# Performance work log

Measured on AMD Instinct MI355X. Metric: run time of the kernel, lower is better.

Reference implementation:

```python
import jax, jax.numpy as jnp
import numpy as np

NUM_ROUTING = 3


def squash(s, axis=-1):
    # squash(s) = |s|^2/(1+|s|^2) * s/|s|  (no epsilon, matching the torch code)
    sq = jnp.sum(s * s, axis=axis, keepdims=True)
    return sq / (1.0 + sq) * (s / jnp.sqrt(sq))


def setup_inputs() -> dict:
    key = jax.random.key(0)
    k1, k2 = jax.random.split(key)
    B, in_dim, in_num = 256, 8, 1152
    out_num, out_dim = 10, 16
    x = jax.random.normal(k1, (B, in_dim, in_num), dtype=jnp.float32)
    W = jax.random.normal(k2, (in_num, out_num, out_dim, in_dim), dtype=jnp.float32)
    return {"x": x, "W": W}


def reference(x, W):
    # x: [B, in_dim, in_num]; W: [in_num(i), out_num(j), out_dim(d), in_dim(c)]
    B = x.shape[0]
    in_num, out_num = W.shape[0], W.shape[1]
    # u_hat[i,j,b,d] = sum_c W[i,j,d,c] * x[b,c,i]
    u_hat = jnp.einsum('ijdc,bci->ijbd', W, x)
    b_ij = jnp.zeros((in_num, out_num), dtype=x.dtype)
    v = None
    for _ in range(NUM_ROUTING):
        # DGL reduce: softmax over the output-capsule axis (bucket dim)
        c = jax.nn.softmax(b_ij, axis=1)                    # [i, j]
        s = jnp.einsum('ij,ijbd->jbd', c, u_hat)            # [j, B, d]
        v = squash(s, axis=2)                               # [j, B, d]
        # edge update: b_ij += mean_b sum_d v[j,b,d] * u_hat[i,j,b,d]
        b_ij = b_ij + jnp.einsum('jbd,ijbd->ij', v, u_hat) / B
    # output: [B, out_num, out_dim, 1]
    return jnp.transpose(v, (1, 0, 2))[..., None]
```

## Files before the change

### kernel.cpp

```cpp
#include <hip/hip_runtime.h>

#define IN_NUM 1152
#define OUT_NUM 10
#define OUT_DIM 16
#define IN_DIM 8
#define NB 256
#define KTOT 9216

#define OFF_SPART 0
#define SZ_SPART (96 * OUT_NUM * OUT_DIM * NB)
#define OFF_VT (OFF_SPART + SZ_SPART)
#define SZ_VT (NB * OUT_NUM * OUT_DIM)
#define OFF_BP (OFF_VT + SZ_VT)
#define SZ_BP (32 * IN_NUM * OUT_NUM)
#define OFF_WT (OFF_BP + SZ_BP)
#define SZ_WT (OUT_NUM * OUT_DIM * IN_DIM * IN_NUM)

#define SMEM_FLOATS 5792

__device__ __forceinline__ void phase1(float* smem, int t, int w, int it,
                                       const float* __restrict__ x, const float* __restrict__ W,
                                       float* __restrict__ Wt,
                                       const float* __restrict__ bp, float* __restrict__ spart) {
    int g8 = w / 80, r = w - g8 * 80;
    int j = r >> 3, isp = g8 * 8 + (r & 7);
    int cch = isp / 12;
    int i0 = (isp - cch * 12) * 96;
    int k0 = isp * 96;
    float (*xt)[260] = (float (*)[260])smem;
    float (*at)[16]  = (float (*)[16])(smem + 4160);
    float* ldc = smem + 5696;
    if (t < 96) {
        float cv;
        if (it == 0) {
            cv = 0.1f;
        } else {
            int i = i0 + t;
            float bt_[OUT_NUM];
#pragma unroll
            for (int jp = 0; jp < OUT_NUM; ++jp) bt_[jp] = 0.f;
#pragma unroll
            for (int row = 0; row < 32; ++row) {
                const float* p = &bp[((size_t)row * IN_NUM + i) * OUT_NUM];
#pragma unroll
                for (int jp = 0; jp < OUT_NUM; ++jp) bt_[jp] += p[jp];
            }
            float m = -1e30f;
#pragma unroll
            for (int jp = 0; jp < OUT_NUM; ++jp) { bt_[jp] *= (1.f / NB); m = fmaxf(m, bt_[jp]); }
            float s = 0.f;
#pragma unroll
            for (int jp = 0; jp < OUT_NUM; ++jp) { bt_[jp] = __expf(bt_[jp] - m); s += bt_[jp]; }
            cv = bt_[j] / s;
        }
        ldc[t] = cv;
    }
    __syncthreads();
    if (it == 0) {
        for (int e = t; e < 1536; e += 128) {
            int d = e / 96, kk = e - d * 96;
            float raw = W[(size_t)(i0 + kk) * 1280 + j * 128 + d * 8 + cch];
            Wt[(size_t)(j * 16 + d) * KTOT + cch * IN_NUM + i0 + kk] = raw;
            at[kk][d] = 0.1f * raw;
        }
    } else {
        for (int e = t; e < 1536; e += 128) {
            int d = e / 96, kk = e - d * 96;
            at[kk][d] = ldc[kk] * Wt[(size_t)(j * 16 + d) * KTOT + cch * IN_NUM + i0 + kk];
        }
    }
    int bb = t & 63, dg = t >> 6;
    int q4 = t & 3, row = t >> 2;
    float acc[32];
#pragma unroll
    for (int q = 0; q < 32; ++q) acc[q] = 0.f;
    for (int ch = 0; ch < 6; ++ch) {
        __syncthreads();
#pragma unroll
        for (int rr = 0; rr < 8; ++rr) {
            int b = rr * 32 + row;
            float4 xv = *reinterpret_cast<const float4*>(
                &x[(size_t)b * KTOT + k0 + ch * 16 + q4 * 4]);
            xt[q4 * 4 + 0][b] = xv.x; xt[q4 * 4 + 1][b] = xv.y;
            xt[q4 * 4 + 2][b] = xv.z; xt[q4 * 4 + 3][b] = xv.w;
        }
        __syncthreads();
#pragma unroll
        for (int kk = 0; kk < 16; ++kk) {
            float4 xv = *reinterpret_cast<const float4*>(&xt[kk][bb * 4]);
            float4 a0 = *reinterpret_cast<const float4*>(&at[ch * 16 + kk][dg * 8]);
            float4 a1 = *reinterpret_cast<const float4*>(&at[ch * 16 + kk][dg * 8 + 4]);
            acc[0]  += a0.x * xv.x; acc[1]  += a0.x * xv.y; acc[2]  += a0.x * xv.z; acc[3]  += a0.x * xv.w;
            acc[4]  += a0.y * xv.x; acc[5]  += a0.y * xv.y; acc[6]  += a0.y * xv.z; acc[7]  += a0.y * xv.w;
            acc[8]  += a0.z * xv.x; acc[9]  += a0.z * xv.y; acc[10] += a0.z * xv.z; acc[11] += a0.z * xv.w;
            acc[12] += a0.w * xv.x; acc[13] += a0.w * xv.y; acc[14] += a0.w * xv.z; acc[15] += a0.w * xv.w;
            acc[16] += a1.x * xv.x; acc[17] += a1.x * xv.y; acc[18] += a1.x * xv.z; acc[19] += a1.x * xv.w;
            acc[20] += a1.y * xv.x; acc[21] += a1.y * xv.y; acc[22] += a1.y * xv.z; acc[23] += a1.y * xv.w;
            acc[24] += a1.z * xv.x; acc[25] += a1.z * xv.y; acc[26] += a1.z * xv.z; acc[27] += a1.z * xv.w;
            acc[28] += a1.w * xv.x; acc[29] += a1.w * xv.y; acc[30] += a1.w * xv.z; acc[31] += a1.w * xv.w;
        }
    }
    float* sp = spart + (size_t)(isp * OUT_NUM + j) * (OUT_DIM * NB);
#pragma unroll
    for (int dd = 0; dd < 8; ++dd) {
        float4 o;
        o.x = acc[dd * 4 + 0]; o.y = acc[dd * 4 + 1];
        o.z = acc[dd * 4 + 2]; o.w = acc[dd * 4 + 3];
        *reinterpret_cast<float4*>(&sp[(dg * 8 + dd) * NB + bb * 4]) = o;
    }
}

__device__ __forceinline__ void phase2(float* smem, int t, int w,
                                       const float* __restrict__ spart, float* __restrict__ dst) {
    float (*red)[32][17] = (float (*)[32][17])smem;
    float (*nrm)[9] = (float (*)[9])(smem + 4352);
    float* cf = smem + 4640;
    int j = w >> 3, bt2 = w & 7;
    int ie = t >> 5, bb = t & 31;
    int b = bt2 * 32 + bb;
    float acc[16];
#pragma unroll
    for (int d = 0; d < 16; ++d) acc[d] = 0.f;
    for (int q = 0; q < 12; ++q) {
        int isp = ie * 12 + q;
        const float* sp = spart + (size_t)(isp * OUT_NUM + j) * (OUT_DIM * NB) + b;
#pragma unroll
        for (int d = 0; d < 16; ++d) acc[d] += sp[d * NB];
    }
#pragma unroll
    for (int d = 0; d < 16; ++d) red[ie][bb][d] = acc[d];
    __syncthreads();
    int bb2 = t >> 3, dp = t & 7;
    float s0 = 0.f, s1 = 0.f;
#pragma unroll
    for (int e = 0; e < 8; ++e) { s0 += red[e][bb2][dp * 2]; s1 += red[e][bb2][dp * 2 + 1]; }
    nrm[bb2][dp] = s0 * s0 + s1 * s1;
    __syncthreads();
    if (t < 32) {
        float qn = 0.f;
#pragma unroll
        for (int d = 0; d < 8; ++d) qn += nrm[t][d];
        cf[t] = qn / ((1.f + qn) * sqrtf(qn));
    }
    __syncthreads();
    float cs = cf[bb2];
    float* o = dst + (size_t)(bt2 * 32 + bb2) * (OUT_NUM * OUT_DIM) + j * OUT_DIM + dp * 2;
    o[0] = s0 * cs;
    o[1] = s1 * cs;
}

__device__ __forceinline__ void phase3(int u, int t, int it,
                                       const float* __restrict__ x, const float* __restrict__ vt,
                                       const float* __restrict__ Wt, float* __restrict__ bp) {
    int kt = u % 36;
    int jq = u / 36;
    int j = jq >> 2, bq = jq & 3;
    int k = kt * 256 + t;
    int c = k / IN_NUM, i = k - c * IN_NUM;
    const float* xk = x + k + (size_t)(bq * 64) * KTOT;
    const float* vjb = vt + (size_t)(bq * 64) * (OUT_NUM * OUT_DIM) + j * OUT_DIM;
    float macc[16];
#pragma unroll
    for (int d = 0; d < 16; ++d) macc[d] = 0.f;
#pragma unroll 8
    for (int b = 0; b < 64; ++b) {
        float xv = xk[(size_t)b * KTOT];
        const float* vb = vjb + (size_t)b * (OUT_NUM * OUT_DIM);
#pragma unroll
        for (int d = 0; d < 16; ++d) macc[d] += vb[d] * xv;
    }
    float bs = 0.f;
#pragma unroll
    for (int d = 0; d < 16; ++d)
        bs += macc[d] * Wt[(size_t)(j * OUT_DIM + d) * KTOT + k];
    size_t idx = (size_t)(bq * 8 + c) * (IN_NUM * OUT_NUM) + (size_t)i * OUT_NUM + j;
    float prev = (it == 0) ? 0.f : bp[idx];
    bp[idx] = prev + bs;
}

__global__ __launch_bounds__(128, 4) void k_p1(const float* __restrict__ x, const float* __restrict__ W,
                                               float* __restrict__ ws, int it) {
    __shared__ float smem[SMEM_FLOATS];
    phase1(smem, threadIdx.x, blockIdx.x, it, x, W, ws + OFF_WT, ws + OFF_BP, ws + OFF_SPART);
}
__global__ __launch_bounds__(256, 4) void k_p2(const float* __restrict__ ws, float* __restrict__ dst) {
    __shared__ float smem[SMEM_FLOATS];
    phase2(smem, threadIdx.x, blockIdx.x, ws + OFF_SPART, dst);
}
__global__ __launch_bounds__(256) void k_p3(const float* __restrict__ x, float* __restrict__ ws, int it) {
    phase3(blockIdx.x, threadIdx.x, it, x, ws + OFF_VT, ws + OFF_WT, ws + OFF_BP);
}

extern "C" void kernel_launch(void* const* d_in, const int* in_sizes, int n_in,
                              void* d_out, int out_size, void* d_ws, size_t ws_size,
                              hipStream_t stream) {
    const float* x = (const float*)d_in[0];
    const float* W = (const float*)d_in[1];
    float* out = (float*)d_out;
    float* ws = (float*)d_ws;

    for (int it = 0; it < 3; ++it) {
        k_p1<<<dim3(960), dim3(128), 0, stream>>>(x, W, ws, it);
        k_p2<<<dim3(80), dim3(256), 0, stream>>>(ws, it == 2 ? out : (ws + OFF_VT));
        if (it < 2) k_p3<<<dim3(1440), dim3(256), 0, stream>>>(x, ws, it);
    }
}
```

Baseline: 126.4 us.

## Fuse squash reduction into agreement kernel, recompute v per block

Merges the partial-sum reduction plus squash (old phase2) with the routing-logit update (old phase3) into one kernel for the first two iterations. Each block redundantly reduces the 96 partial sums for its 64-batch slice and output capsule, squashes them into shared memory, and then computes agreement for 1536 k values per block. The dot with v is now taken before multiplying by x, and W is kept in registers. This removes one launch per iteration and the v round trip through global memory, at the cost of redundant spart reads across the six k-slices and heavy register use.

```diff
diff --git a/kernel.cpp b/kernel.cpp
--- a/kernel.cpp
+++ b/kernel.cpp
@@ -9,9 +9,7 @@
 
 #define OFF_SPART 0
 #define SZ_SPART (96 * OUT_NUM * OUT_DIM * NB)
-#define OFF_VT (OFF_SPART + SZ_SPART)
-#define SZ_VT (NB * OUT_NUM * OUT_DIM)
-#define OFF_BP (OFF_VT + SZ_VT)
+#define OFF_BP (OFF_SPART + SZ_SPART)
 #define SZ_BP (32 * IN_NUM * OUT_NUM)
 #define OFF_WT (OFF_BP + SZ_BP)
 #define SZ_WT (OUT_NUM * OUT_DIM * IN_DIM * IN_NUM)
@@ -149,33 +147,78 @@
     o[1] = s1 * cs;
 }
 
-__device__ __forceinline__ void phase3(int u, int t, int it,
-                                       const float* __restrict__ x, const float* __restrict__ vt,
-                                       const float* __restrict__ Wt, float* __restrict__ bp) {
-    int kt = u % 36;
-    int jq = u / 36;
-    int j = jq >> 2, bq = jq & 3;
-    int k = kt * 256 + t;
-    int c = k / IN_NUM, i = k - c * IN_NUM;
-    const float* xk = x + k + (size_t)(bq * 64) * KTOT;
-    const float* vjb = vt + (size_t)(bq * 64) * (OUT_NUM * OUT_DIM) + j * OUT_DIM;
-    float macc[16];
-#pragma unroll
-    for (int d = 0; d < 16; ++d) macc[d] = 0.f;
-#pragma unroll 8
+__global__ __launch_bounds__(256) void k_pB(const float* __restrict__ x,
+                                            float* __restrict__ ws, int it) {
+    __shared__ float vlds[64][20];
+    __shared__ float sq[4][64];
+    __shared__ float cf[64];
+    const float* spart = ws + OFF_SPART;
+    const float* Wt = ws + OFF_WT;
+    float* bp = ws + OFF_BP;
+    int u = blockIdx.x, t = threadIdx.x;
+    int g = u / 80, r = u - g * 80;
+    int j = r >> 3, e = r & 7, m = g * 8 + e;
+    int bq = m / 6, ks = m - bq * 6;
+    int dq = t >> 6, bb = t & 63;
+
+    float sacc[4] = {0.f, 0.f, 0.f, 0.f};
+    const float* spb = spart + ((size_t)j * OUT_DIM + dq * 4) * NB + bq * 64 + bb;
+#pragma unroll 4
+    for (int isp = 0; isp < 96; ++isp) {
+        const float* sp = spb + (size_t)isp * (OUT_NUM * OUT_DIM * NB);
+        sacc[0] += sp[0]; sacc[1] += sp[NB]; sacc[2] += sp[2 * NB]; sacc[3] += sp[3 * NB];
+    }
+    sq[dq][bb] = sacc[0] * sacc[0] + sacc[1] * sacc[1] + sacc[2] * sacc[2] + sacc[3] * sacc[3];
+#pragma unroll
+    for (int dd = 0; dd < 4; ++dd) vlds[bb][dq * 4 + dd] = sacc[dd];
+    __syncthreads();
+    if (t < 64) {
+        float qn = sq[0][t] + sq[1][t] + sq[2][t] + sq[3][t];
+        cf[t] = qn / ((1.f + qn) * sqrtf(qn));
+    }
+    __syncthreads();
+    {
+        float c_ = cf[bb];
+#pragma unroll
+        for (int dd = 0; dd < 4; ++dd) vlds[bb][dq * 4 + dd] = sacc[dd] * c_;
+    }
+    __syncthreads();
+
+    int kbase = ks * 1536 + t;
+    float wt[6][16];
+#pragma unroll
+    for (int kt = 0; kt < 6; ++kt) {
+        int k = kbase + kt * 256;
+#pragma unroll
+        for (int d = 0; d < 16; ++d)
+            wt[kt][d] = Wt[(size_t)(j * OUT_DIM + d) * KTOT + k];
+    }
+    float bs[6] = {0.f, 0.f, 0.f, 0.f, 0.f, 0.f};
+    const float* xb = x + (size_t)(bq * 64) * KTOT + kbase;
+#pragma unroll 2
     for (int b = 0; b < 64; ++b) {
-        float xv = xk[(size_t)b * KTOT];
-        const float* vb = vjb + (size_t)b * (OUT_NUM * OUT_DIM);
-#pragma unroll
-        for (int d = 0; d < 16; ++d) macc[d] += vb[d] * xv;
-    }
-    float bs = 0.f;
-#pragma unroll
-    for (int d = 0; d < 16; ++d)
-        bs += macc[d] * Wt[(size_t)(j * OUT_DIM + d) * KTOT + k];
-    size_t idx = (size_t)(bq * 8 + c) * (IN_NUM * OUT_NUM) + (size_t)i * OUT_NUM + j;
-    float prev = (it == 0) ? 0.f : bp[idx];
-    bp[idx] = prev + bs;
+        float4 v0 = *reinterpret_cast<const float4*>(&vlds[b][0]);
+        float4 v1 = *reinterpret_cast<const float4*>(&vlds[b][4]);
+        float4 v2 = *reinterpret_cast<const float4*>(&vlds[b][8]);
+        float4 v3 = *reinterpret_cast<const float4*>(&vlds[b][12]);
+        const float* xrow = xb + (size_t)b * KTOT;
+#pragma unroll
+        for (int kt = 0; kt < 6; ++kt) {
+            float dot = wt[kt][0] * v0.x + wt[kt][1] * v0.y + wt[kt][2] * v0.z + wt[kt][3] * v0.w
+                      + wt[kt][4] * v1.x + wt[kt][5] * v1.y + wt[kt][6] * v1.z + wt[kt][7] * v1.w
+                      + wt[kt][8] * v2.x + wt[kt][9] * v2.y + wt[kt][10] * v2.z + wt[kt][11] * v2.w
+                      + wt[kt][12] * v3.x + wt[kt][13] * v3.y + wt[kt][14] * v3.z + wt[kt][15] * v3.w;
+            bs[kt] += xrow[kt * 256] * dot;
+        }
+    }
+#pragma unroll
+    for (int kt = 0; kt < 6; ++kt) {
+        int k = kbase + kt * 256;
+        int c = k / IN_NUM, i = k - c * IN_NUM;
+        size_t idx = (size_t)(bq * 8 + c) * (IN_NUM * OUT_NUM) + (size_t)i * OUT_NUM + j;
+        float prev = (it == 0) ? 0.f : bp[idx];
+        bp[idx] = prev + bs[kt];
+    }
 }
 
 __global__ __launch_bounds__(128, 4) void k_p1(const float* __restrict__ x, const float* __restrict__ W,
@@ -186,9 +229,6 @@
 __global__ __launch_bounds__(256, 4) void k_p2(const float* __restrict__ ws, float* __restrict__ dst) {
     __shared__ float smem[SMEM_FLOATS];
     phase2(smem, threadIdx.x, blockIdx.x, ws + OFF_SPART, dst);
-}
-__global__ __launch_bounds__(256) void k_p3(const float* __restrict__ x, float* __restrict__ ws, int it) {
-    phase3(blockIdx.x, threadIdx.x, it, x, ws + OFF_VT, ws + OFF_WT, ws + OFF_BP);
 }
 
 extern "C" void kernel_launch(void* const* d_in, const int* in_sizes, int n_in,
@@ -201,7 +241,9 @@
 
     for (int it = 0; it < 3; ++it) {
         k_p1<<<dim3(960), dim3(128), 0, stream>>>(x, W, ws, it);
-        k_p2<<<dim3(80), dim3(256), 0, stream>>>(ws, it == 2 ? out : (ws + OFF_VT));
-        if (it < 2) k_p3<<<dim3(1440), dim3(256), 0, stream>>>(x, ws, it);
-    }
-}
+        if (it < 2)
+            k_pB<<<dim3(240), dim3(256), 0, stream>>>(x, ws, it);
+        else
+            k_p2<<<dim3(80), dim3(256), 0, stream>>>(ws, out);
+    }
+}
```

Measured after the change: 153.0 us. 1.21x slower.
